# Kernel optimization log

Hardware: AMD Instinct MI355X
Metric: run time of the kernel (lower is better)

The kernel has to match this reference:

```python
import jax, jax.numpy as jnp
import numpy as np

MARGIN = 0.3
N, D = 8192, 256
NUM_IDS = 1000


def setup_inputs() -> dict:
    key = jax.random.key(0)
    k1, k2 = jax.random.split(key)
    inputs = jax.random.normal(k1, (N, D), dtype=jnp.float32)
    targets = jax.random.randint(k2, (N,), 0, NUM_IDS, dtype=jnp.int64)
    return {"inputs": inputs, "targets": targets}


def reference(inputs, targets):
    # sim_mat[i, j] = <x_i, x_j>
    sim = jnp.matmul(inputs, inputs.T)  # [n, n]
    same = targets[:, None] == targets[None, :]  # [n, n] bool
    # positives: same label AND sim < 1 (note: strict; diagonal included only if ||x||^2 < 1)
    pos_mask = same & (sim < 1.0)
    # negatives: different label AND sim > margin
    neg_mask = (~same) & (sim > MARGIN)
    pos_loss = jnp.sum(jnp.where(pos_mask, 1.0 - sim, 0.0), axis=1)  # [n]
    neg_loss = jnp.sum(jnp.where(neg_mask, sim, 0.0), axis=1)  # [n]
    n = inputs.shape[0]
    return jnp.sum(pos_loss + neg_loss) / n
```

## Files before the change

kernel.cpp:

```cpp
#include <hip/hip_runtime.h>
#include <hip/hip_bf16.h>


#define MARGINF 0.3f

typedef __attribute__((ext_vector_type(8))) short short8x;
typedef __attribute__((ext_vector_type(16))) float f32x16;

__device__ __forceinline__ unsigned short f2bf(float f) {
    unsigned int u = __float_as_uint(f);
    unsigned int r = (u + 0x7fffu + ((u >> 16) & 1u)) >> 16;
    return (unsigned short)r;
}

__global__ void __launch_bounds__(256) convert_k(const float* __restrict__ x,
                                                 unsigned short* __restrict__ xb) {
    int i = blockIdx.x * 256 + threadIdx.x;
    const float4* p = reinterpret_cast<const float4*>(x) + (size_t)i * 2;
    float4 a = p[0];
    float4 b = p[1];
    short8x o;
    o[0] = (short)f2bf(a.x); o[1] = (short)f2bf(a.y);
    o[2] = (short)f2bf(a.z); o[3] = (short)f2bf(a.w);
    o[4] = (short)f2bf(b.x); o[5] = (short)f2bf(b.y);
    o[6] = (short)f2bf(b.z); o[7] = (short)f2bf(b.w);
    reinterpret_cast<short8x*>(xb)[i] = o;
}

__global__ void __launch_bounds__(256, 3) gemm_loss_k(const unsigned short* __restrict__ xb,
                                                      const int* __restrict__ tg,
                                                      double* __restrict__ partials) {
    const int p = blockIdx.x;
    int bi = (int)(64.5f - sqrtf(64.5f * 64.5f - 2.0f * (float)p));
    if (bi < 0) bi = 0;
    if (bi > 63) bi = 63;
    while (bi > 0 && (bi * (129 - bi)) / 2 > p) --bi;
    while (((bi + 1) * (128 - bi)) / 2 <= p) ++bi;
    const int bj = bi + (p - (bi * (129 - bi)) / 2);

    __shared__ __align__(16) char ldsb[3 * 16384];
    __shared__ int lti[128];
    __shared__ int ltj[128];
    __shared__ float redbuf[4];

    const int tid  = threadIdx.x;
    const int lane = tid & 63;
    const int wid  = tid >> 6;
    const int wr   = wid >> 1;
    const int wc   = wid & 1;

    if (tid < 128)       lti[tid]        = tg[bi * 128 + tid];
    else                 ltj[tid - 128]  = tg[bj * 128 + (tid - 128)];
    __syncthreads();

    const char* aBase = (const char*)(xb + (size_t)bi * 128 * 256);
    const char* bBase = (const char*)(xb + (size_t)bj * 128 * 256);

    const int srow0  = wid * 16 + (lane >> 2);
    const int schunk = (((lane & 3) ^ ((lane >> 3) & 3))) << 4;

    const int l31 = lane & 31;
    const int hi  = lane >> 5;
    const int swz = (l31 >> 1) & 3;
    int offA[2][2], offB[2][2];
#pragma unroll
    for (int fm = 0; fm < 2; ++fm)
#pragma unroll
        for (int ks = 0; ks < 2; ++ks)
            offA[fm][ks] = (wr * 64 + fm * 32 + l31) * 64 + ((((ks << 1) | hi) ^ swz) << 4);
#pragma unroll
    for (int fn = 0; fn < 2; ++fn)
#pragma unroll
        for (int ks = 0; ks < 2; ++ks)
            offB[fn][ks] = 8192 + (wc * 64 + fn * 32 + l31) * 64 + ((((ks << 1) | hi) ^ swz) << 4);

    f32x16 acc00 = {}, acc01 = {}, acc10 = {}, acc11 = {};

#define STAGE_KT(BUF, T) do {                                                        \
    _Pragma("unroll")                                                                \
    for (int i_ = 0; i_ < 2; ++i_) {                                                 \
        const int r_ = i_ * 64 + srow0;                                              \
        const char* sa_ = aBase + (size_t)r_ * 512 + (T) * 64 + schunk;              \
        const char* sb_ = bBase + (size_t)r_ * 512 + (T) * 64 + schunk;              \
        __builtin_amdgcn_global_load_lds(                                            \
            (const __attribute__((address_space(1))) unsigned int*)sa_,              \
            (__attribute__((address_space(3))) unsigned int*)(ldsb + (BUF) * 16384 + i_ * 4096 + wid * 1024), \
            16, 0, 0);                                                               \
        __builtin_amdgcn_global_load_lds(                                            \
            (const __attribute__((address_space(1))) unsigned int*)sb_,              \
            (__attribute__((address_space(3))) unsigned int*)(ldsb + (BUF) * 16384 + 8192 + i_ * 4096 + wid * 1024), \
            16, 0, 0);                                                               \
    }                                                                                \
} while (0)

#define GEMM_ITER(T, BUF, VMSTR, DOSTAGE) do {                                       \
    asm volatile("s_waitcnt vmcnt(" VMSTR ")" ::: "memory");                         \
    __builtin_amdgcn_s_barrier();                     \
    const char* lb_ = ldsb + (BUF) * 16384;                                          \
    short8x a0k0 = *(const short8x*)(lb_ + offA[0][0]);                              \
    short8x a1k0 = *(const short8x*)(lb_ + offA[1][0]);                              \
    short8x b0k0 = *(const short8x*)(lb_ + offB[0][0]);                              \
    short8x b1k0 = *(const short8x*)(lb_ + offB[1][0]);                              \
    short8x a0k1 = *(const short8x*)(lb_ + offA[0][1]);                              \
    short8x a1k1 = *(const short8x*)(lb_ + offA[1][1]);                              \
    short8x b0k1 = *(const short8x*)(lb_ + offB[0][1]);                              \
    short8x b1k1 = *(const short8x*)(lb_ + offB[1][1]);                              \
    asm volatile("s_waitcnt lgkmcnt(0)" ::: "memory");                               \
    __builtin_amdgcn_sched_barrier(0);                                               \
    __builtin_amdgcn_s_barrier();                    \
    if (DOSTAGE) STAGE_KT(BUF, (T) + 3);                    \
    __builtin_amdgcn_s_setprio(1);                                                   \
    acc00 = __builtin_amdgcn_mfma_f32_32x32x16_bf16(a0k0, b0k0, acc00, 0, 0, 0);     \
    acc01 = __builtin_amdgcn_mfma_f32_32x32x16_bf16(a0k0, b1k0, acc01, 0, 0, 0);     \
    acc10 = __builtin_amdgcn_mfma_f32_32x32x16_bf16(a1k0, b0k0, acc10, 0, 0, 0);     \
    acc11 = __builtin_amdgcn_mfma_f32_32x32x16_bf16(a1k0, b1k0, acc11, 0, 0, 0);     \
    acc00 = __builtin_amdgcn_mfma_f32_32x32x16_bf16(a0k1, b0k1, acc00, 0, 0, 0);     \
    acc01 = __builtin_amdgcn_mfma_f32_32x32x16_bf16(a0k1, b1k1, acc01, 0, 0, 0);     \
    acc10 = __builtin_amdgcn_mfma_f32_32x32x16_bf16(a1k1, b0k1, acc10, 0, 0, 0);     \
    acc11 = __builtin_amdgcn_mfma_f32_32x32x16_bf16(a1k1, b1k1, acc11, 0, 0, 0);     \
    __builtin_amdgcn_s_setprio(0);                                                   \
} while (0)

    STAGE_KT(0, 0);
    STAGE_KT(1, 1);
    STAGE_KT(2, 2);

    GEMM_ITER(0, 0, "8", 1);
    GEMM_ITER(1, 1, "8", 1);
    GEMM_ITER(2, 2, "8", 1);
    GEMM_ITER(3, 0, "8", 1);
    GEMM_ITER(4, 1, "8", 1);
    GEMM_ITER(5, 2, "8", 0);
    GEMM_ITER(6, 0, "4", 0);
    GEMM_ITER(7, 1, "0", 0);

#undef GEMM_ITER
#undef STAGE_KT

    const int hi4 = hi * 4;
    const int col_l = l31;
    int tjv[2];
#pragma unroll
    for (int fn = 0; fn < 2; ++fn) tjv[fn] = ltj[wc * 64 + fn * 32 + col_l];

    float lsum = 0.f;
    const f32x16* accs[4] = { &acc00, &acc01, &acc10, &acc11 };

    if (bi != bj) {
#pragma unroll
        for (int fm = 0; fm < 2; ++fm) {
#pragma unroll
            for (int fn = 0; fn < 2; ++fn) {
                const f32x16& A = *accs[fm * 2 + fn];
                const int tj = tjv[fn];
#pragma unroll
                for (int r = 0; r < 16; ++r) {
                    const int row_l = (r & 3) + 8 * (r >> 2) + hi4;
                    const int ti = lti[wr * 64 + fm * 32 + row_l];
                    const float s = A[r];
                    const float posv = fmaxf(1.0f - s, 0.0f);
                    const float negv = (s > MARGINF) ? s : 0.0f;
                    lsum += (ti == tj) ? posv : negv;
                }
            }
        }
        lsum *= 2.0f;
    } else {
#pragma unroll
        for (int fm = 0; fm < 2; ++fm) {
#pragma unroll
            for (int fn = 0; fn < 2; ++fn) {
                const f32x16& A = *accs[fm * 2 + fn];
                const int tj = tjv[fn];
                const int cl = wc * 64 + fn * 32 + col_l;
#pragma unroll
                for (int r = 0; r < 16; ++r) {
                    const int row_l = (r & 3) + 8 * (r >> 2) + hi4;
                    const int rl = wr * 64 + fm * 32 + row_l;
                    const int ti = lti[rl];
                    const float s = A[r];
                    const float posv = fmaxf(1.0f - s, 0.0f);
                    const float negv = (s > MARGINF) ? s : 0.0f;
                    const float c = (ti == tj) ? posv : negv;
                    const float w = (cl > rl) ? 2.0f : ((cl == rl) ? 1.0f : 0.0f);
                    lsum += w * c;
                }
            }
        }
    }

#pragma unroll
    for (int mask = 1; mask < 64; mask <<= 1) lsum += __shfl_xor(lsum, mask, 64);
    if (lane == 0) redbuf[wid] = lsum;
    __syncthreads();
    if (tid == 0)
        partials[p] = (double)(redbuf[0] + redbuf[1] + redbuf[2] + redbuf[3]);
}

__global__ void __launch_bounds__(256) finalize_k(const double* __restrict__ partials,
                                                  float* __restrict__ out) {
    double s = 0.0;
    for (int i = threadIdx.x; i < 2080; i += 256) s += partials[i];
#pragma unroll
    for (int mask = 1; mask < 64; mask <<= 1) s += __shfl_xor(s, mask, 64);
    __shared__ double red[4];
    const int wid = threadIdx.x >> 6;
    if ((threadIdx.x & 63) == 0) red[wid] = s;
    __syncthreads();
    if (threadIdx.x == 0)
        out[0] = (float)((red[0] + red[1] + red[2] + red[3]) / 8192.0);
}

extern "C" void kernel_launch(void* const* d_in, const int* in_sizes, int n_in,
                              void* d_out, int out_size, void* d_ws, size_t ws_size,
                              hipStream_t stream) {
    (void)in_sizes; (void)n_in; (void)out_size; (void)ws_size;
    const float* x  = (const float*)d_in[0];
    const int*   tg = (const int*)d_in[1];
    float* out = (float*)d_out;

    double* partials   = (double*)d_ws;
    unsigned short* xb = (unsigned short*)((char*)d_ws + 32768);

    convert_k<<<1024, 256, 0, stream>>>(x, xb);
    gemm_loss_k<<<2080, 256, 0, stream>>>(xb, tg, partials);
    finalize_k<<<1, 256, 0, stream>>>(partials, out);
}
```

Baseline: 89.50 us.

## Split loss into label-free negative sum plus per-label same-pair correction kernel

The GEMM epilogue now applies only the negative-margin term to every pair, with no label lookups and no triangular weighting. A new kernel groups rows by label, recomputes the dot products of same-label pairs, and adds the positive term while subtracting the negative term. This drops the LDS label loads and per-element branching from the hot epilogue. In exchange it adds a kernel launch and a scan of all targets for each label. It also hardcodes 1000 labels and caps each label at 96 members.

```diff
diff --git a/kernel.cpp b/kernel.cpp
--- a/kernel.cpp
+++ b/kernel.cpp
@@ -28,7 +28,6 @@
 }
 
 __global__ void __launch_bounds__(256, 3) gemm_loss_k(const unsigned short* __restrict__ xb,
-                                                      const int* __restrict__ tg,
                                                       double* __restrict__ partials) {
     const int p = blockIdx.x;
     int bi = (int)(64.5f - sqrtf(64.5f * 64.5f - 2.0f * (float)p));
@@ -39,8 +38,6 @@
     const int bj = bi + (p - (bi * (129 - bi)) / 2);
 
     __shared__ __align__(16) char ldsb[3 * 16384];
-    __shared__ int lti[128];
-    __shared__ int ltj[128];
     __shared__ float redbuf[4];
 
     const int tid  = threadIdx.x;
@@ -48,10 +45,6 @@
     const int wid  = tid >> 6;
     const int wr   = wid >> 1;
     const int wc   = wid & 1;
-
-    if (tid < 128)       lti[tid]        = tg[bi * 128 + tid];
-    else                 ltj[tid - 128]  = tg[bj * 128 + (tid - 128)];
-    __syncthreads();
 
     const char* aBase = (const char*)(xb + (size_t)bi * 128 * 256);
     const char* bBase = (const char*)(xb + (size_t)bj * 128 * 256);
@@ -137,70 +130,73 @@
 #undef GEMM_ITER
 #undef STAGE_KT
 
-    const int hi4 = hi * 4;
-    const int col_l = l31;
-    int tjv[2];
-#pragma unroll
-    for (int fn = 0; fn < 2; ++fn) tjv[fn] = ltj[wc * 64 + fn * 32 + col_l];
-
     float lsum = 0.f;
-    const f32x16* accs[4] = { &acc00, &acc01, &acc10, &acc11 };
-
-    if (bi != bj) {
-#pragma unroll
-        for (int fm = 0; fm < 2; ++fm) {
-#pragma unroll
-            for (int fn = 0; fn < 2; ++fn) {
-                const f32x16& A = *accs[fm * 2 + fn];
-                const int tj = tjv[fn];
-#pragma unroll
-                for (int r = 0; r < 16; ++r) {
-                    const int row_l = (r & 3) + 8 * (r >> 2) + hi4;
-                    const int ti = lti[wr * 64 + fm * 32 + row_l];
-                    const float s = A[r];
-                    const float posv = fmaxf(1.0f - s, 0.0f);
-                    const float negv = (s > MARGINF) ? s : 0.0f;
-                    lsum += (ti == tj) ? posv : negv;
-                }
+#pragma unroll
+    for (int r = 0; r < 16; ++r) {
+        float s;
+        s = acc00[r]; lsum += (s > MARGINF) ? s : 0.0f;
+        s = acc01[r]; lsum += (s > MARGINF) ? s : 0.0f;
+        s = acc10[r]; lsum += (s > MARGINF) ? s : 0.0f;
+        s = acc11[r]; lsum += (s > MARGINF) ? s : 0.0f;
+    }
+    if (bi != bj) lsum *= 2.0f;
+
+#pragma unroll
+    for (int mask = 1; mask < 64; mask <<= 1) lsum += __shfl_xor(lsum, mask, 64);
+    if (lane == 0) redbuf[wid] = lsum;
+    __syncthreads();
+    if (tid == 0)
+        partials[p] = (double)(redbuf[0] + redbuf[1] + redbuf[2] + redbuf[3]);
+}
+
+__global__ void __launch_bounds__(256) samepair_k(const unsigned short* __restrict__ xb,
+                                                  const int* __restrict__ tg,
+                                                  double* __restrict__ partials2) {
+    const int lbl = blockIdx.x;
+    __shared__ int idx[96];
+    __shared__ int cnt;
+    __shared__ double dred[4];
+    if (threadIdx.x == 0) cnt = 0;
+    __syncthreads();
+    for (int i = threadIdx.x; i < 8192; i += 256)
+        if (tg[i] == lbl) { int q = atomicAdd(&cnt, 1); if (q < 96) idx[q] = i; }
+    __syncthreads();
+    int c = cnt; if (c > 96) c = 96;
+
+    double dsum = 0.0;
+    for (int t = threadIdx.x; t < c * c; t += 256) {
+        const int i = idx[t / c], j = idx[t % c];
+        const short8x* xi = (const short8x*)(xb + (size_t)i * 256);
+        const short8x* xj = (const short8x*)(xb + (size_t)j * 256);
+        float s = 0.f;
+#pragma unroll 4
+        for (int q = 0; q < 32; ++q) {
+            short8x a = xi[q], b = xj[q];
+#pragma unroll
+            for (int e = 0; e < 8; ++e) {
+                float fa = __uint_as_float(((unsigned int)(unsigned short)a[e]) << 16);
+                float fb = __uint_as_float(((unsigned int)(unsigned short)b[e]) << 16);
+                s = fmaf(fa, fb, s);
             }
         }
-        lsum *= 2.0f;
-    } else {
-#pragma unroll
-        for (int fm = 0; fm < 2; ++fm) {
-#pragma unroll
-            for (int fn = 0; fn < 2; ++fn) {
-                const f32x16& A = *accs[fm * 2 + fn];
-                const int tj = tjv[fn];
-                const int cl = wc * 64 + fn * 32 + col_l;
-#pragma unroll
-                for (int r = 0; r < 16; ++r) {
-                    const int row_l = (r & 3) + 8 * (r >> 2) + hi4;
-                    const int rl = wr * 64 + fm * 32 + row_l;
-                    const int ti = lti[rl];
-                    const float s = A[r];
-                    const float posv = fmaxf(1.0f - s, 0.0f);
-                    const float negv = (s > MARGINF) ? s : 0.0f;
-                    const float c = (ti == tj) ? posv : negv;
-                    const float w = (cl > rl) ? 2.0f : ((cl == rl) ? 1.0f : 0.0f);
-                    lsum += w * c;
-                }
-            }
-        }
+        const float posv = (s < 1.0f) ? (1.0f - s) : 0.0f;
+        const float negv = (s > MARGINF) ? s : 0.0f;
+        dsum += (double)(posv - negv);
     }
 
 #pragma unroll
-    for (int mask = 1; mask < 64; mask <<= 1) lsum += __shfl_xor(lsum, mask, 64);
-    if (lane == 0) redbuf[wid] = lsum;
-    __syncthreads();
-    if (tid == 0)
-        partials[p] = (double)(redbuf[0] + redbuf[1] + redbuf[2] + redbuf[3]);
+    for (int mask = 1; mask < 64; mask <<= 1) dsum += __shfl_xor(dsum, mask, 64);
+    const int wid = threadIdx.x >> 6;
+    if ((threadIdx.x & 63) == 0) dred[wid] = dsum;
+    __syncthreads();
+    if (threadIdx.x == 0)
+        partials2[lbl] = dred[0] + dred[1] + dred[2] + dred[3];
 }
 
 __global__ void __launch_bounds__(256) finalize_k(const double* __restrict__ partials,
                                                   float* __restrict__ out) {
     double s = 0.0;
-    for (int i = threadIdx.x; i < 2080; i += 256) s += partials[i];
+    for (int i = threadIdx.x; i < 3080; i += 256) s += partials[i];
 #pragma unroll
     for (int mask = 1; mask < 64; mask <<= 1) s += __shfl_xor(s, mask, 64);
     __shared__ double red[4];
@@ -220,9 +216,11 @@
     float* out = (float*)d_out;
 
     double* partials   = (double*)d_ws;
+    double* partials2  = (double*)d_ws + 2080;
     unsigned short* xb = (unsigned short*)((char*)d_ws + 32768);
 
     convert_k<<<1024, 256, 0, stream>>>(x, xb);
-    gemm_loss_k<<<2080, 256, 0, stream>>>(xb, tg, partials);
+    gemm_loss_k<<<2080, 256, 0, stream>>>(xb, partials);
+    samepair_k<<<1000, 256, 0, stream>>>(xb, tg, partials2);
     finalize_k<<<1, 256, 0, stream>>>(partials, out);
 }
```

Measured after the change: 110.4 us. 23.4% more time.
